# Optimization experiments

Hardware: AMD Instinct MI355X
Metric: run time of the kernel (lower is better)

The kernel has to match this reference:

```python
import jax, jax.numpy as jnp
import numpy as np

B, CI, HI, WI = 64, 3, 96, 96
G = 8
HG, WG = 16, 16
HIDLIN = 512
SIGMA_BOOST = 2.0
EPS = 1e-7
HID = (HI // 4 // 2) * (WI // 4 // 2) * 128  # 12*12*128 = 18432


def _conv(x, w, b):
    # NCHW conv, 3x3, padding 1 (matches nn.Conv2d(kernel_size=3, padding=1))
    y = jax.lax.conv_general_dilated(x, w, (1, 1), ((1, 1), (1, 1)),
                                     dimension_numbers=('NCHW', 'OIHW', 'NCHW'))
    return y + b[None, :, None, None]


def _maxpool(x, k):
    return jax.lax.reduce_window(x, -jnp.inf, jax.lax.max,
                                 (1, 1, k, k), (1, 1, k, k), 'VALID')


def setup_inputs() -> dict:
    key = jax.random.key(0)
    ks = jax.random.split(key, 22)

    def w(k, shape, fan_in):
        return jax.random.normal(k, shape, jnp.float32) * np.float32(1.0 / np.sqrt(fan_in))

    return {
        'image': jax.random.normal(ks[0], (B, CI, HI, WI), jnp.float32),
        'noise': jax.random.normal(ks[1], (B * G, 2), jnp.float32),
        # conv block 1
        'w1a': w(ks[2], (32, CI, 3, 3), CI * 9), 'b1a': jnp.zeros((32,), jnp.float32),
        'w1b': w(ks[3], (32, 32, 3, 3), 32 * 9), 'b1b': jnp.zeros((32,), jnp.float32),
        # conv block 2
        'w2a': w(ks[4], (64, 32, 3, 3), 32 * 9), 'b2a': jnp.zeros((64,), jnp.float32),
        'w2b': w(ks[5], (64, 64, 3, 3), 64 * 9), 'b2b': jnp.zeros((64,), jnp.float32),
        # conv block 3
        'w3a': w(ks[6], (128, 64, 3, 3), 64 * 9), 'b3a': jnp.zeros((128,), jnp.float32),
        'w3b': w(ks[7], (128, 128, 3, 3), 128 * 9), 'b3b': jnp.zeros((128,), jnp.float32),
        # linear head (weights stored (in, out))
        'wl1': w(ks[8], (HID, HIDLIN), HID), 'bl1': jnp.zeros((HIDLIN,), jnp.float32),
        'wl2': w(ks[9], (HIDLIN, HIDLIN), HIDLIN), 'bl2': jnp.zeros((HIDLIN,), jnp.float32),
        'wl3': w(ks[10], (HIDLIN, G * 3), HIDLIN), 'bl3': jnp.zeros((G * 3,), jnp.float32),
    }


def reference(image, noise, w1a, b1a, w1b, b1b, w2a, b2a, w2b, b2b,
              w3a, b3a, w3b, b3b, wl1, bl1, wl2, bl2, wl3, bl3):
    # --- preprocess CNN ---
    x = jax.nn.relu(_conv(image, w1a, b1a))
    x = jax.nn.relu(_conv(x, w1b, b1b))
    x = _maxpool(x, 4)
    x = jax.nn.relu(_conv(x, w2a, b2a))
    x = jax.nn.relu(_conv(x, w2b, b2b))
    x = _maxpool(x, 2)
    x = jax.nn.relu(_conv(x, w3a, b3a))
    x = jax.nn.relu(_conv(x, w3b, b3b))
    x = x.reshape(B, -1)                      # Flatten (C,H,W order, like torch .view)
    x = jax.nn.relu(x @ wl1 + bl1)
    x = jax.nn.relu(x @ wl2 + bl2)            # Linear(HIDLIN,HIDLIN) then the extra ReLU
    prep = (x @ wl3 + bl3).reshape(B * G, 3)  # (b*g, 3)

    means = prep[:, :2]                        # (b*g, 2) raw means
    sraw = prep[:, 2]
    # sparse.transform_sigmas: softplus(s + SIGMA_BOOST) + eps, scaled per spatial dim
    sig = jax.nn.softplus(sraw + SIGMA_BOOST) + EPS
    sigmas = sig[:, None] * jnp.array([HI - 1, WI - 1], jnp.float32)  # (b*g, 2)

    # Normal(means, sigmas).sample() -> reparameterized but detached (torch .sample())
    sample = jax.lax.stop_gradient(means + sigmas * noise)
    # sparse.transform_means over size (hi-hg, wi-wg): sigmoid * (size-1), then round
    msize = jnp.array([HI - HG - 1, WI - WG - 1], jnp.float32)
    pts = jnp.round(jax.nn.sigmoid(sample) * msize).astype(jnp.int32).reshape(B, G, 2)

    # glimpse extraction: the original's b*g python slicing loop -> vmapped dynamic_slice
    src = jax.lax.stop_gradient(image)  # original slices image.data (no grad)

    def ext_one(img, p):
        return jax.lax.dynamic_slice(img, (jnp.int32(0), p[0], p[1]), (CI, HG, WG))

    result = jax.vmap(lambda img, ps: jax.vmap(lambda p: ext_one(img, p))(ps))(src, pts)
    # result: (B, G, CI, HG, WG)
    return result, means.reshape(B, G, 2), sigmas.reshape(B, G, 2)
```

## Files before the change

kernel.cpp:

```cpp
#include <hip/hip_runtime.h>
#include <math.h>

constexpr int BB  = 64;
constexpr int CIc = 3;
constexpr int HIc = 96, WIc = 96;
constexpr int Gc  = 8, HGc = 16, WGc = 16;
constexpr int HIDc = 18432;
constexpr int HIDLINc = 512;

using short8 = __attribute__((ext_vector_type(8))) short;
using s4     = __attribute__((ext_vector_type(4))) short;
using f32x16 = __attribute__((ext_vector_type(16))) float;

__device__ inline unsigned short bfr(float f) {
    unsigned int u = __float_as_uint(f);
    u = (u + 0x7FFFu + ((u >> 16) & 1u)) >> 16;
    return (unsigned short)u;
}
__device__ inline float ubf(unsigned short s) {
    return __uint_as_float(((unsigned int)s) << 16);
}
__device__ inline void tsplit(float v, unsigned short& H, unsigned short& M,
                              unsigned short& L) {
    unsigned int u = __float_as_uint(v);
    H = (unsigned short)(u >> 16);
    float r1 = v - __uint_as_float(u & 0xFFFF0000u);
    unsigned int u1 = __float_as_uint(r1);
    M = (unsigned short)(u1 >> 16);
    float r2 = r1 - __uint_as_float(u1 & 0xFFFF0000u);
    L = (unsigned short)(__float_as_uint(r2) >> 16);
}

__device__ __attribute__((aligned(16))) unsigned short g_wh[9216];
__device__ __attribute__((aligned(16))) unsigned short g_wm[9216];
__device__ __attribute__((aligned(16))) unsigned short g_wl[9216];

__device__ __attribute__((aligned(16))) unsigned short g_w1ah[1536];
__device__ __attribute__((aligned(16))) unsigned short g_w1am[1536];
__device__ __attribute__((aligned(16))) unsigned short g_w1al[1536];

__device__ __attribute__((aligned(16))) unsigned short g_wph[276480];
__device__ __attribute__((aligned(16))) unsigned short g_wpm[276480];
__device__ __attribute__((aligned(16))) unsigned short g_wpl[276480];

__device__ inline void packN_one(const float* __restrict__ w, int CIN, int ofs,
                                 int idx)
{
    int chsz = 288 * CIN;
    int chunk = idx / chsz;
    int t = idx - chunk * chsz;
    int s = t >> 9;
    int rr = t & 511;
    int g = rr >> 8, oc32 = (rr >> 3) & 31, j = rr & 7;
    int nc16 = CIN / 16;
    int tap = s / nc16, c16 = s % nc16;
    int ci = c16 * 16 + g * 8 + j;
    int oc = chunk * 32 + oc32;
    float v = w[((size_t)oc * CIN + ci) * 9 + tap];
    unsigned short h = bfr(v);
    float r1 = v - ubf(h);
    unsigned short m = bfr(r1);
    g_wph[ofs + idx] = h; g_wpm[ofs + idx] = m; g_wpl[ofs + idx] = bfr(r1 - ubf(m));
}

__device__ inline void bz_one(unsigned short* __restrict__ Xh,
                              unsigned short* __restrict__ Xm,
                              unsigned short* __restrict__ Xl,
                              int PAD, int C, int idx)
{
    int RING = 4 * PAD - 4;
    int ci = idx % C;
    int cell = (idx / C) % RING;
    int b = idx / (C * RING);
    int y, x;
    if (cell < PAD)          { y = 0;       x = cell; }
    else if (cell < 2 * PAD) { y = PAD - 1; x = cell - PAD; }
    else { int t = cell - 2 * PAD; y = 1 + (t >> 1); x = (t & 1) ? PAD - 1 : 0; }
    size_t a = ((size_t)(b * PAD + y) * PAD + x) * C + ci;
    Xh[a] = 0; Xm[a] = 0; Xl[a] = 0;
}

__global__ void prep_all(const float* __restrict__ w1a, const float* __restrict__ w1b,
                         const float* __restrict__ w2a, const float* __restrict__ w2b,
                         const float* __restrict__ w3a, const float* __restrict__ w3b,
                         const float* __restrict__ image,
                         unsigned short* Ih, unsigned short* Im, unsigned short* Il,
                         unsigned short* X2h, unsigned short* X2m, unsigned short* X2l,
                         unsigned short* X3h, unsigned short* X3m, unsigned short* X3l,
                         unsigned short* X4h, unsigned short* X4m, unsigned short* X4l,
                         unsigned short* X5h, unsigned short* X5m, unsigned short* X5l)
{
    int idx = blockIdx.x * 256 + threadIdx.x;
    if (idx < 9216) {
        int j = idx & 7, oc = (idx >> 3) & 31, g = (idx >> 8) & 1, s = idx >> 9;
        int ci = 16 * (s & 1) + 8 * g + j;
        int tap = s >> 1;
        float v = w1b[(oc * 32 + ci) * 9 + tap];
        unsigned short h = bfr(v);
        float r1 = v - ubf(h);
        unsigned short m = bfr(r1);
        g_wh[idx] = h; g_wm[idx] = m; g_wl[idx] = bfr(r1 - ubf(m));
    } else if (idx < 27648) {
        packN_one(w2a, 32, 0, idx - 9216);
    } else if (idx < 64512) {
        packN_one(w2b, 64, 18432, idx - 27648);
    } else if (idx < 138240) {
        packN_one(w3a, 64, 55296, idx - 64512);
    } else if (idx < 285696) {
        packN_one(w3b, 128, 129024, idx - 138240);
    } else if (idx < 287232) {
        int i2 = idx - 285696;
        int j = i2 & 7, oc = (i2 >> 3) & 31, gg = (i2 >> 8) & 1, s = i2 >> 9;
        int k = s * 16 + gg * 8 + j;
        int tap = k >> 2, ci = k & 3;
        float v = (tap < 9 && ci < 3) ? w1a[((size_t)oc * 3 + ci) * 9 + tap] : 0.0f;
        unsigned short h = bfr(v);
        float r1 = v - ubf(h);
        unsigned short m = bfr(r1);
        g_w1ah[i2] = h; g_w1am[i2] = m; g_w1al[i2] = bfr(r1 - ubf(m));
    } else if (idx < 927232) {
        int c = idx - 287232;
        int x = c % 100;
        int t = c / 100;
        int y = t % 100;
        int b = t / 100;
        s4 H = {0, 0, 0, 0}, M = {0, 0, 0, 0}, L = {0, 0, 0, 0};
        if (y >= 2 && y < 98 && x >= 2 && x < 98) {
#pragma unroll
            for (int ci = 0; ci < 3; ++ci) {
                float v = image[((size_t)(b * 3 + ci) * 96 + (y - 2)) * 96 + (x - 2)];
                unsigned short hh, mm, ll;
                tsplit(v, hh, mm, ll);
                H[ci] = (short)hh; M[ci] = (short)mm; L[ci] = (short)ll;
            }
        }
        *(s4*)(Ih + (size_t)c * 4) = H;
        *(s4*)(Im + (size_t)c * 4) = M;
        *(s4*)(Il + (size_t)c * 4) = L;
    } else {
        int c = idx - 927232;
        if (c < 204800)        bz_one(X2h, X2m, X2l, 26, 32, c);
        else if (c < 614400)   bz_one(X3h, X3m, X3l, 26, 64, c - 204800);
        else if (c < 827392)   bz_one(X4h, X4m, X4l, 14, 64, c - 614400);
        else if (c < 1253376)  bz_one(X5h, X5m, X5l, 14, 128, c - 827392);
    }
}

__global__ __launch_bounds__(256, 5)
void conv1ab(const unsigned short* __restrict__ Ih,
             const unsigned short* __restrict__ Im,
             const unsigned short* __restrict__ Il,
             const float* __restrict__ b1a, const float* __restrict__ b1b,
             unsigned short* __restrict__ X2h, unsigned short* __restrict__ X2m,
             unsigned short* __restrict__ X2l)
{
    const int id    = blockIdx.x;
    const int xcd   = id & 7;
    const int local = id >> 3;
    const int gblk  = xcd * 576 + local;
    const int b  = gblk / 72;
    const int r  = gblk % 72;
    const int yq = r / 3;
    const int xt = r % 3;

    const int tid = threadIdx.x;
    const int wave = tid >> 6, lane = tid & 63;
    const int col = lane & 31, g = lane >> 5;

    __shared__ __align__(16) short s_hml[3][6][34][20];
    __shared__ float s_pool[4][8][2][16];
    __shared__ float s_b1a[32], s_b1b[32];
    if (tid < 32) { s_b1a[tid] = b1a[tid]; s_b1b[tid] = b1b[tid]; }
    __syncthreads();

    auto convA = [&](int tile, f32x16& acc) {
        int p = tile * 32 + col;
        int pc = p < 204 ? p : 203;
        int lr = pc / 34, lc = pc - (pc / 34) * 34;
        const size_t ibase =
            ((size_t)(b * 100 + 4 * yq + lr) * 100 + 32 * xt + lc) * 4;
#pragma unroll
        for (int s = 0; s < 3; ++s) {
            int tap0 = 4 * s + 2 * g; if (tap0 > 8) tap0 = 8;
            int tap1 = 4 * s + 2 * g + 1; if (tap1 > 8) tap1 = 8;
            int o0 = ((tap0 / 3) * 100 + tap0 % 3) * 4;
            int o1 = ((tap1 / 3) * 100 + tap1 % 3) * 4;
            s4 h0 = *(const s4*)(Ih + ibase + o0);
            s4 h1 = *(const s4*)(Ih + ibase + o1);
            s4 m0 = *(const s4*)(Im + ibase + o0);
            s4 m1 = *(const s4*)(Im + ibase + o1);
            s4 l0 = *(const s4*)(Il + ibase + o0);
            s4 l1 = *(const s4*)(Il + ibase + o1);
            short8 bh = __builtin_shufflevector(h0, h1, 0, 1, 2, 3, 4, 5, 6, 7);
            short8 bm = __builtin_shufflevector(m0, m1, 0, 1, 2, 3, 4, 5, 6, 7);
            short8 bl = __builtin_shufflevector(l0, l1, 0, 1, 2, 3, 4, 5, 6, 7);
            const int aidx = s * 512 + g * 256 + col * 8;
            short8 ah = *(const short8*)(g_w1ah + aidx);
            short8 am = *(const short8*)(g_w1am + aidx);
            short8 al = *(const short8*)(g_w1al + aidx);
            acc = __builtin_amdgcn_mfma_f32_32x32x16_bf16(ah, bh, acc, 0, 0, 0);
            acc = __builtin_amdgcn_mfma_f32_32x32x16_bf16(ah, bm, acc, 0, 0, 0);
            acc = __builtin_amdgcn_mfma_f32_32x32x16_bf16(am, bh, acc, 0, 0, 0);
            acc = __builtin_amdgcn_mfma_f32_32x32x16_bf16(am, bm, acc, 0, 0, 0);
            acc = __builtin_amdgcn_mfma_f32_32x32x16_bf16(al, bh, acc, 0, 0, 0);
            acc = __builtin_amdgcn_mfma_f32_32x32x16_bf16(ah, bl, acc, 0, 0, 0);
            acc = __builtin_amdgcn_mfma_f32_32x32x16_bf16(am, bl, acc, 0, 0, 0);
            acc = __builtin_amdgcn_mfma_f32_32x32x16_bf16(al, bm, acc, 0, 0, 0);
        }
    };

    f32x16 accA0 = {0,0,0,0,0,0,0,0,0,0,0,0,0,0,0,0};
    f32x16 accA1 = {0,0,0,0,0,0,0,0,0,0,0,0,0,0,0,0};
    convA(wave * 2, accA0);
    if (wave != 3) convA(wave * 2 + 1, accA1);

    f32x16 acc0 = {0,0,0,0,0,0,0,0,0,0,0,0,0,0,0,0};
    f32x16 acc1 = {0,0,0,0,0,0,0,0,0,0,0,0,0,0,0,0};

#pragma unroll
    for (int half = 0; half < 2; ++half) {
        if (half) __syncthreads();

#pragma unroll
        for (int t = 0; t < 2; ++t) {
            int tile = wave * 2 + t;
            int p = tile * 32 + col;
            if (tile < 7 && p < 204) {
                const f32x16& A = t ? accA1 : accA0;
                int lr = p / 34, lc = p - (p / 34) * 34;
                int gr = 4 * yq - 1 + lr, gc = 32 * xt - 1 + lc;
                bool valid = (gr >= 0 && gr < 96 && gc >= 0 && gc < 96);
                s4 H0, M0, L0, H1, M1, L1;
#pragma unroll
                for (int i = 0; i < 4; ++i) {
                    float v0 = valid ? fmaxf(A[8 * half + i] +
                                     s_b1a[16 * half + 4 * g + i], 0.0f) : 0.0f;
                    float v1 = valid ? fmaxf(A[8 * half + 4 + i] +
                                     s_b1a[16 * half + 8 + 4 * g + i], 0.0f) : 0.0f;
                    unsigned short hh, mm, ll;
                    tsplit(v0, hh, mm, ll);
                    H0[i] = (short)hh; M0[i] = (short)mm; L0[i] = (short)ll;
                    tsplit(v1, hh, mm, ll);
                    H1[i] = (short)hh; M1[i] = (short)mm; L1[i] = (short)ll;
                }
                *(s4*)&s_hml[0][lr][lc][4 * g]     = H0;
                *(s4*)&s_hml[0][lr][lc][8 + 4 * g] = H1;
                *(s4*)&s_hml[1][lr][lc][4 * g]     = M0;
                *(s4*)&s_hml[1][lr][lc][8 + 4 * g] = M1;
                *(s4*)&s_hml[2][lr][lc][4 * g]     = L0;
                *(s4*)&s_hml[2][lr][lc][8 + 4 * g] = L1;
            }
        }
        __syncthreads();

        __builtin_amdgcn_s_setprio(1);
#pragma unroll
        for (int tap = 0; tap < 9; ++tap) {
            const int s = tap * 2 + half;
            const int dy = tap / 3, dx = tap % 3;
            const int aidx = s * 512 + g * 256 + col * 8;

            s4 a0 = *(const s4*)(&s_hml[0][wave + dy][col + dx][g * 8]);
            s4 a1 = *(const s4*)(&s_hml[0][wave + dy][col + dx][g * 8 + 4]);
            s4 b0 = *(const s4*)(&s_hml[1][wave + dy][col + dx][g * 8]);
            s4 b1 = *(const s4*)(&s_hml[1][wave + dy][col + dx][g * 8 + 4]);
            s4 c0 = *(const s4*)(&s_hml[2][wave + dy][col + dx][g * 8]);
            s4 c1 = *(const s4*)(&s_hml[2][wave + dy][col + dx][g * 8 + 4]);

            short8 bh = __builtin_shufflevector(a0, a1, 0, 1, 2, 3, 4, 5, 6, 7);
            short8 bm = __builtin_shufflevector(b0, b1, 0, 1, 2, 3, 4, 5, 6, 7);
            short8 bl = __builtin_shufflevector(c0, c1, 0, 1, 2, 3, 4, 5, 6, 7);

            short8 ah = *(const short8*)(g_wh + aidx);
            short8 am = *(const short8*)(g_wm + aidx);
            short8 al = *(const short8*)(g_wl + aidx);

            acc0 = __builtin_amdgcn_mfma_f32_32x32x16_bf16(ah, bh, acc0, 0, 0, 0);
            acc1 = __builtin_amdgcn_mfma_f32_32x32x16_bf16(ah, bm, acc1, 0, 0, 0);
            acc0 = __builtin_amdgcn_mfma_f32_32x32x16_bf16(am, bh, acc0, 0, 0, 0);
            acc1 = __builtin_amdgcn_mfma_f32_32x32x16_bf16(am, bm, acc1, 0, 0, 0);
            acc0 = __builtin_amdgcn_mfma_f32_32x32x16_bf16(al, bh, acc0, 0, 0, 0);
            acc1 = __builtin_amdgcn_mfma_f32_32x32x16_bf16(ah, bl, acc1, 0, 0, 0);
        }
        __builtin_amdgcn_s_setprio(0);
    }
    __syncthreads();

#pragma unroll
    for (int rr = 0; rr < 16; ++rr) {
        int ocr = (rr & 3) + 8 * (rr >> 2) + 4 * g;
        float v = fmaxf(acc0[rr] + acc1[rr] + s_b1b[ocr], 0.0f);
        v = fmaxf(v, __shfl_xor(v, 1));
        v = fmaxf(v, __shfl_xor(v, 2));
        if ((col & 3) == 0) s_pool[wave][col >> 2][g][rr] = v;
    }
    __syncthreads();

    {
        int oc = tid & 31, pc = tid >> 5;
        if (pc < 8) {
            int gg = (oc >> 2) & 1;
            int rr = (oc & 3) + (((oc >> 3) & 3) << 2);
            float mv = s_pool[0][pc][gg][rr];
            mv = fmaxf(mv, s_pool[1][pc][gg][rr]);
            mv = fmaxf(mv, s_pool[2][pc][gg][rr]);
            mv = fmaxf(mv, s_pool[3][pc][gg][rr]);
            unsigned short h, m, l;
            tsplit(mv, h, m, l);
            size_t oa = ((size_t)(b * 26 + yq + 1) * 26 + xt * 8 + pc + 1) * 32 + oc;
            X2h[oa] = h; X2m[oa] = m; X2l[oa] = l;
        }
    }
}

template<int CIN, int HW, int NCHUNK, int OUTMODE>
__global__ __launch_bounds__(256)
void convN_mfma(const unsigned short* __restrict__ Xh,
                const unsigned short* __restrict__ Xm,
                const unsigned short* __restrict__ Xl,
                int wofs, const float* __restrict__ bias,
                unsigned short* __restrict__ Yh,
                unsigned short* __restrict__ Ym,
                unsigned short* __restrict__ Yl,
                float* __restrict__ Yf)
{
    constexpr int PAD = HW + 2;
    constexpr int NC16 = CIN / 16;
    constexpr int CHSZ = 288 * CIN;
    constexpr int COUT = NCHUNK * 32;

    const int tid = threadIdx.x;
    const int cpx = gridDim.x >> 3;
    const int blk = (blockIdx.x & 7) * cpx + (blockIdx.x >> 3);
    const int wid = blk * 4 + (tid >> 6);
    const int lane = tid & 63;
    const int col = lane & 31, g = lane >> 5;

    const int chunk = wid % NCHUNK;
    const int wt = wid / NCHUNK;
    const int P = wt * 32 + col;
    const int b = P / (HW * HW);
    const int rem = P - b * (HW * HW);
    const int y = rem / HW, x = rem - y * HW;

    const size_t ib = ((size_t)(b * PAD + y) * PAD + x) * CIN + g * 8;
    const int wbase = wofs + chunk * CHSZ;

    f32x16 acc0 = {0,0,0,0,0,0,0,0,0,0,0,0,0,0,0,0};
    f32x16 acc1 = {0,0,0,0,0,0,0,0,0,0,0,0,0,0,0,0};

#pragma unroll
    for (int tap = 0; tap < 9; ++tap) {
        const int dy = tap / 3, dx = tap % 3;
        for (int c16 = 0; c16 < NC16; ++c16) {
            const int s = tap * NC16 + c16;
            const int aidx = wbase + s * 512 + g * 256 + col * 8;
            const size_t xo = ib + (size_t)((dy * PAD + dx) * CIN + c16 * 16);
            short8 ah = *(const short8*)(g_wph + aidx);
            short8 am = *(const short8*)(g_wpm + aidx);
            short8 al = *(const short8*)(g_wpl + aidx);
            short8 bh = *(const short8*)(Xh + xo);
            short8 bm = *(const short8*)(Xm + xo);
            short8 bl = *(const short8*)(Xl + xo);
            acc0 = __builtin_amdgcn_mfma_f32_32x32x16_bf16(ah, bh, acc0, 0, 0, 0);
            acc1 = __builtin_amdgcn_mfma_f32_32x32x16_bf16(ah, bm, acc1, 0, 0, 0);
            acc0 = __builtin_amdgcn_mfma_f32_32x32x16_bf16(am, bh, acc0, 0, 0, 0);
            acc1 = __builtin_amdgcn_mfma_f32_32x32x16_bf16(am, bm, acc1, 0, 0, 0);
            acc0 = __builtin_amdgcn_mfma_f32_32x32x16_bf16(al, bh, acc0, 0, 0, 0);
            acc1 = __builtin_amdgcn_mfma_f32_32x32x16_bf16(ah, bl, acc1, 0, 0, 0);
        }
    }

    if constexpr (OUTMODE == 0) {
        const size_t obase =
            ((size_t)(b * PAD + y + 1) * PAD + (x + 1)) * COUT + chunk * 32;
#pragma unroll
        for (int q = 0; q < 4; ++q) {
            s4 H, M, L;
#pragma unroll
            for (int i = 0; i < 4; ++i) {
                int r = q * 4 + i;
                int ocr = i + 8 * q + 4 * g;
                float v = fmaxf(acc0[r] + acc1[r] + bias[chunk * 32 + ocr], 0.0f);
                unsigned short h, m, l;
                tsplit(v, h, m, l);
                H[i] = (short)h; M[i] = (short)m; L[i] = (short)l;
            }
            *(s4*)(Yh + obase + 8 * q + 4 * g) = H;
            *(s4*)(Ym + obase + 8 * q + 4 * g) = M;
            *(s4*)(Yl + obase + 8 * q + 4 * g) = L;
        }
    } else {
#pragma unroll
        for (int r = 0; r < 16; ++r) {
            int ocr = chunk * 32 + (r & 3) + 8 * (r >> 2) + 4 * g;
            float v = fmaxf(acc0[r] + acc1[r] + bias[ocr], 0.0f);
            Yf[((size_t)(b * COUT + ocr) * HW + y) * HW + x] = v;
        }
    }
}

__global__ __launch_bounds__(256)
void pool2_pack(const float* __restrict__ t2,
                unsigned short* __restrict__ X4h,
                unsigned short* __restrict__ X4m,
                unsigned short* __restrict__ X4l)
{
    int idx = blockIdx.x * 256 + threadIdx.x;
    constexpr int TOT = BB * 144 * 64;
    if (idx >= TOT) return;
    int oc = idx & 63;
    int p = (idx >> 6) % 144;
    int b = idx / (144 * 64);
    int y = p / 12, x = p % 12;
    const float* src = t2 + ((size_t)(b * 64 + oc) * 24 + 2 * y) * 24 + 2 * x;
    float v = fmaxf(fmaxf(src[0], src[1]), fmaxf(src[24], src[25]));
    unsigned short h, m, l;
    tsplit(v, h, m, l);
    size_t oa = ((size_t)(b * 14 + y + 1) * 14 + x + 1) * 64 + oc;
    X4h[oa] = h; X4m[oa] = m; X4l[oa] = l;
}

constexpr int KSPLIT = 64;
__global__ __launch_bounds__(256)
void lin1_partial(const float* __restrict__ x, const float* __restrict__ w,
                  float* __restrict__ partial)
{
    const int j  = threadIdx.x % 64;
    const int bg = threadIdx.x / 64;
    const int jBase = blockIdx.x * 64;
    const int k  = blockIdx.y;
    const int i0 = k * 288;

    __shared__ float s_x[32][68];

    float acc[16];
#pragma unroll
    for (int u = 0; u < 16; ++u) acc[u] = 0.0f;

    for (int ib = 0; ib < 288; ib += 32) {
        __syncthreads();
        {
            int lb = threadIdx.x / 4;
            int lo = (threadIdx.x % 4) * 8;
            const float* src = x + (size_t)lb * HIDc + i0 + ib + lo;
            float4 a0 = *(const float4*)(src);
            float4 a1 = *(const float4*)(src + 4);
            float tmp[8] = {a0.x, a0.y, a0.z, a0.w, a1.x, a1.y, a1.z, a1.w};
#pragma unroll
            for (int r = 0; r < 8; ++r) s_x[lo + r][lb] = tmp[r];
        }
        __syncthreads();

        for (int ii = 0; ii < 32; ++ii) {
            float wv = w[(size_t)(i0 + ib + ii) * HIDLINc + jBase + j];
            const float4* xp = (const float4*)&s_x[ii][bg * 16];
            float4 x0 = xp[0], x1 = xp[1], x2 = xp[2], x3 = xp[3];
            acc[0]  = fmaf(x0.x, wv, acc[0]);
            acc[1]  = fmaf(x0.y, wv, acc[1]);
            acc[2]  = fmaf(x0.z, wv, acc[2]);
            acc[3]  = fmaf(x0.w, wv, acc[3]);
            acc[4]  = fmaf(x1.x, wv, acc[4]);
            acc[5]  = fmaf(x1.y, wv, acc[5]);
            acc[6]  = fmaf(x1.z, wv, acc[6]);
            acc[7]  = fmaf(x1.w, wv, acc[7]);
            acc[8]  = fmaf(x2.x, wv, acc[8]);
            acc[9]  = fmaf(x2.y, wv, acc[9]);
            acc[10] = fmaf(x2.z, wv, acc[10]);
            acc[11] = fmaf(x2.w, wv, acc[11]);
            acc[12] = fmaf(x3.x, wv, acc[12]);
            acc[13] = fmaf(x3.y, wv, acc[13]);
            acc[14] = fmaf(x3.z, wv, acc[14]);
            acc[15] = fmaf(x3.w, wv, acc[15]);
        }
    }

#pragma unroll
    for (int u = 0; u < 16; ++u) {
        int b = bg * 16 + u;
        partial[((size_t)k * 64 + b) * HIDLINc + jBase + j] = acc[u];
    }
}

__global__ void lin1_reduce(const float* __restrict__ partial,
                            const float* __restrict__ bias,
                            float* __restrict__ x1)
{
    int idx = blockIdx.x * blockDim.x + threadIdx.x;
    if (idx >= 64 * HIDLINc) return;
    int j = idx % HIDLINc;
    float s = 0.0f;
    for (int k = 0; k < KSPLIT; ++k)
        s += partial[(size_t)k * 64 * HIDLINc + idx];
    x1[idx] = fmaxf(s + bias[j], 0.0f);
}

__global__ __launch_bounds__(256)
void lin2_k(const float* __restrict__ x1, const float* __restrict__ w,
            const float* __restrict__ bias, float* __restrict__ x2)
{
    const int j  = threadIdx.x % 64;
    const int bl = threadIdx.x / 64;
    const int jBase = blockIdx.x * 64;
    const int b = blockIdx.y * 4 + bl;

    __shared__ float s_x[4][HIDLINc];
    for (int idx = threadIdx.x; idx < 4 * HIDLINc; idx += 256)
        s_x[idx / HIDLINc][idx % HIDLINc] =
            x1[(size_t)(blockIdx.y * 4 + idx / HIDLINc) * HIDLINc + idx % HIDLINc];
    __syncthreads();

    float acc = 0.0f;
    for (int i = 0; i < HIDLINc; ++i)
        acc = fmaf(s_x[bl][i], w[(size_t)i * HIDLINc + jBase + j], acc);
    x2[(size_t)b * HIDLINc + jBase + j] = fmaxf(acc + bias[jBase + j], 0.0f);
}

__global__ void lin3_k(const float* __restrict__ x2, const float* __restrict__ w,
                       const float* __restrict__ bias, float* __restrict__ prep)
{
    int idx = blockIdx.x * blockDim.x + threadIdx.x;
    if (idx >= 64 * 24) return;
    int j = idx % 24, b = idx / 24;
    float acc = bias[j];
    for (int i = 0; i < HIDLINc; ++i)
        acc = fmaf(x2[(size_t)b * HIDLINc + i], w[i * 24 + j], acc);
    prep[idx] = acc;
}

__global__ void head_k(const float* __restrict__ prep, const float* __restrict__ noise,
                       float* __restrict__ outMeans, float* __restrict__ outSigmas,
                       int* __restrict__ pts)
{
    int id = blockIdx.x * blockDim.x + threadIdx.x;
    if (id >= BB * Gc) return;
    float m0 = prep[id * 3 + 0];
    float m1 = prep[id * 3 + 1];
    float sraw = prep[id * 3 + 2];
    float s = sraw + 2.0f;
    float sig = fmaxf(s, 0.0f) + log1pf(expf(-fabsf(s)));
    sig += 1e-7f;
    float sg = sig * 95.0f;
    outMeans[id * 2 + 0] = m0;
    outMeans[id * 2 + 1] = m1;
    outSigmas[id * 2 + 0] = sg;
    outSigmas[id * 2 + 1] = sg;
    float sa0 = m0 + sg * noise[id * 2 + 0];
    float sa1 = m1 + sg * noise[id * 2 + 1];
    float t0 = 1.0f / (1.0f + expf(-sa0));
    float t1 = 1.0f / (1.0f + expf(-sa1));
    pts[id * 2 + 0] = (int)rintf(t0 * 79.0f);
    pts[id * 2 + 1] = (int)rintf(t1 * 79.0f);
}

__global__ __launch_bounds__(256)
void patch_k(const float* __restrict__ image, const int* __restrict__ pts,
             float* __restrict__ outR)
{
    int id = blockIdx.x;
    int b = id / Gc;
    int p0 = pts[id * 2 + 0];
    int p1 = pts[id * 2 + 1];
    for (int idx = threadIdx.x; idx < CIc * HGc * WGc; idx += 256) {
        int c = idx / (HGc * WGc), rem = idx % (HGc * WGc);
        int hh = rem / WGc, ww = rem % WGc;
        outR[(size_t)id * (CIc * HGc * WGc) + idx] =
            image[((size_t)(b * CIc + c) * HIc + p0 + hh) * WIc + p1 + ww];
    }
}

extern "C" void kernel_launch(void* const* d_in, const int* in_sizes, int n_in,
                              void* d_out, int out_size, void* d_ws, size_t ws_size,
                              hipStream_t stream)
{
    const float* image = (const float*)d_in[0];
    const float* noise = (const float*)d_in[1];
    const float* w1a = (const float*)d_in[2];
    const float* b1a = (const float*)d_in[3];
    const float* w1b = (const float*)d_in[4];
    const float* b1b = (const float*)d_in[5];
    const float* w2a = (const float*)d_in[6];
    const float* b2a = (const float*)d_in[7];
    const float* w2b = (const float*)d_in[8];
    const float* b2b = (const float*)d_in[9];
    const float* w3a = (const float*)d_in[10];
    const float* b3a = (const float*)d_in[11];
    const float* w3b = (const float*)d_in[12];
    const float* b3b = (const float*)d_in[13];
    const float* wl1 = (const float*)d_in[14];
    const float* bl1 = (const float*)d_in[15];
    const float* wl2 = (const float*)d_in[16];
    const float* bl2 = (const float*)d_in[17];
    const float* wl3 = (const float*)d_in[18];
    const float* bl3 = (const float*)d_in[19];

    float* out = (float*)d_out;
    float* ws  = (float*)d_ws;

    unsigned short* X2h = (unsigned short*)(ws + 29884416);
    unsigned short* X2m = (unsigned short*)(ws + 30670848);
    unsigned short* X2l = (unsigned short*)(ws + 31457280);
    unsigned short* X3h = (unsigned short*)(ws);
    unsigned short* X3m = (unsigned short*)(ws + 1572864);
    unsigned short* X3l = (unsigned short*)(ws + 3145728);
    float*  t2  = ws + 4718592;
    unsigned short* X4h = (unsigned short*)(ws + 7340032);
    unsigned short* X4m = (unsigned short*)(ws + 7864320);
    unsigned short* X4l = (unsigned short*)(ws + 8388608);
    unsigned short* X5h = (unsigned short*)(ws + 8912896);
    unsigned short* X5m = (unsigned short*)(ws + 11010048);
    unsigned short* X5l = (unsigned short*)(ws + 12058624);
    float*  t5  = ws + 13107200;
    float*  part= ws + 14680064;
    float*  x1  = ws + 16777216;
    float*  x2  = x1 + 32768;
    float*  prep= x2 + 32768;
    int*    pts = (int*)(prep + 2048);
    unsigned short* Ih = (unsigned short*)(ws + 18874368);
    unsigned short* Im = (unsigned short*)(ws + 20447232);
    unsigned short* Il = (unsigned short*)(ws + 22020096);

    prep_all<<<8518, 256, 0, stream>>>(w1a, w1b, w2a, w2b, w3a, w3b, image,
                                       Ih, Im, Il,
                                       X2h, X2m, X2l, X3h, X3m, X3l,
                                       X4h, X4m, X4l, X5h, X5m, X5l);

    conv1ab<<<4608, 256, 0, stream>>>(Ih, Im, Il, b1a, b1b, X2h, X2m, X2l);

    convN_mfma<32, 24, 2, 0><<<576, 256, 0, stream>>>(
        X2h, X2m, X2l, 0, b2a, X3h, X3m, X3l, nullptr);
    convN_mfma<64, 24, 2, 1><<<576, 256, 0, stream>>>(
        X3h, X3m, X3l, 18432, b2b, nullptr, nullptr, nullptr, t2);
    pool2_pack<<<2304, 256, 0, stream>>>(t2, X4h, X4m, X4l);
    convN_mfma<64, 12, 4, 0><<<288, 256, 0, stream>>>(
        X4h, X4m, X4l, 55296, b3a, X5h, X5m, X5l, nullptr);
    convN_mfma<128, 12, 4, 1><<<288, 256, 0, stream>>>(
        X5h, X5m, X5l, 129024, b3b, nullptr, nullptr, nullptr, t5);

    lin1_partial<<<dim3(8, KSPLIT), 256, 0, stream>>>(t5, wl1, part);
    lin1_reduce<<<(64 * HIDLINc + 255) / 256, 256, 0, stream>>>(part, bl1, x1);
    lin2_k<<<dim3(8, 16), 256, 0, stream>>>(x1, wl2, bl2, x2);
    lin3_k<<<6, 256, 0, stream>>>(x2, wl3, bl3, prep);
    head_k<<<2, 256, 0, stream>>>(prep, noise,
                                  out + (size_t)BB * Gc * CIc * HGc * WGc,
                                  out + (size_t)BB * Gc * CIc * HGc * WGc + BB * Gc * 2,
                                  pts);
    patch_k<<<BB * Gc, 256, 0, stream>>>(image, pts, out);
}
```

Baseline: 354.7 us.

## Trim conv1a split-bf16 MFMA terms, use one-wave conv blocks, fuse lin3 with head

Conv1a's emulated-fp32 product drops the two mid×low MFMA cross terms, leaving six bf16 MFMAs per step instead of eight. The convN_mfma kernels move from 256-thread blocks with four waves to 64-thread single-wave blocks, with four times as many blocks and the same per-wave work. lin3 and the sampling head are fused into one per-batch kernel that keeps the hidden vector and prep values in shared memory, removing one launch and a global round-trip. Dropping the cross terms lowers conv1a precision, which could shift the rounded glimpse coordinates.

```diff
diff --git a/kernel.cpp b/kernel.cpp
--- a/kernel.cpp
+++ b/kernel.cpp
@@ -204,8 +204,6 @@
             acc = __builtin_amdgcn_mfma_f32_32x32x16_bf16(am, bm, acc, 0, 0, 0);
             acc = __builtin_amdgcn_mfma_f32_32x32x16_bf16(al, bh, acc, 0, 0, 0);
             acc = __builtin_amdgcn_mfma_f32_32x32x16_bf16(ah, bl, acc, 0, 0, 0);
-            acc = __builtin_amdgcn_mfma_f32_32x32x16_bf16(am, bl, acc, 0, 0, 0);
-            acc = __builtin_amdgcn_mfma_f32_32x32x16_bf16(al, bm, acc, 0, 0, 0);
         }
     };
 
@@ -314,7 +312,7 @@
 }
 
 template<int CIN, int HW, int NCHUNK, int OUTMODE>
-__global__ __launch_bounds__(256)
+__global__ __launch_bounds__(64)
 void convN_mfma(const unsigned short* __restrict__ Xh,
                 const unsigned short* __restrict__ Xm,
                 const unsigned short* __restrict__ Xl,
@@ -329,12 +327,10 @@
     constexpr int CHSZ = 288 * CIN;
     constexpr int COUT = NCHUNK * 32;
 
-    const int tid = threadIdx.x;
+    const int lane = threadIdx.x & 63;
+    const int col = lane & 31, g = lane >> 5;
     const int cpx = gridDim.x >> 3;
-    const int blk = (blockIdx.x & 7) * cpx + (blockIdx.x >> 3);
-    const int wid = blk * 4 + (tid >> 6);
-    const int lane = tid & 63;
-    const int col = lane & 31, g = lane >> 5;
+    const int wid = (blockIdx.x & 7) * cpx + (blockIdx.x >> 3);
 
     const int chunk = wid % NCHUNK;
     const int wt = wid / NCHUNK;
@@ -516,41 +512,49 @@
     x2[(size_t)b * HIDLINc + jBase + j] = fmaxf(acc + bias[jBase + j], 0.0f);
 }
 
-__global__ void lin3_k(const float* __restrict__ x2, const float* __restrict__ w,
-                       const float* __restrict__ bias, float* __restrict__ prep)
-{
-    int idx = blockIdx.x * blockDim.x + threadIdx.x;
-    if (idx >= 64 * 24) return;
-    int j = idx % 24, b = idx / 24;
-    float acc = bias[j];
-    for (int i = 0; i < HIDLINc; ++i)
-        acc = fmaf(x2[(size_t)b * HIDLINc + i], w[i * 24 + j], acc);
-    prep[idx] = acc;
-}
-
-__global__ void head_k(const float* __restrict__ prep, const float* __restrict__ noise,
-                       float* __restrict__ outMeans, float* __restrict__ outSigmas,
-                       int* __restrict__ pts)
-{
-    int id = blockIdx.x * blockDim.x + threadIdx.x;
-    if (id >= BB * Gc) return;
-    float m0 = prep[id * 3 + 0];
-    float m1 = prep[id * 3 + 1];
-    float sraw = prep[id * 3 + 2];
-    float s = sraw + 2.0f;
-    float sig = fmaxf(s, 0.0f) + log1pf(expf(-fabsf(s)));
-    sig += 1e-7f;
-    float sg = sig * 95.0f;
-    outMeans[id * 2 + 0] = m0;
-    outMeans[id * 2 + 1] = m1;
-    outSigmas[id * 2 + 0] = sg;
-    outSigmas[id * 2 + 1] = sg;
-    float sa0 = m0 + sg * noise[id * 2 + 0];
-    float sa1 = m1 + sg * noise[id * 2 + 1];
-    float t0 = 1.0f / (1.0f + expf(-sa0));
-    float t1 = 1.0f / (1.0f + expf(-sa1));
-    pts[id * 2 + 0] = (int)rintf(t0 * 79.0f);
-    pts[id * 2 + 1] = (int)rintf(t1 * 79.0f);
+__global__ __launch_bounds__(256)
+void lin3head_k(const float* __restrict__ x2, const float* __restrict__ w,
+                const float* __restrict__ bias, const float* __restrict__ noise,
+                float* __restrict__ outMeans, float* __restrict__ outSigmas,
+                int* __restrict__ pts)
+{
+    const int b = blockIdx.x;
+    const int tid = threadIdx.x;
+    __shared__ float s_x[HIDLINc];
+    __shared__ float s_prep[24];
+
+    for (int i = tid; i < HIDLINc; i += 256)
+        s_x[i] = x2[(size_t)b * HIDLINc + i];
+    __syncthreads();
+
+    if (tid < 24) {
+        float acc = bias[tid];
+        for (int i = 0; i < HIDLINc; ++i)
+            acc = fmaf(s_x[i], w[i * 24 + tid], acc);
+        s_prep[tid] = acc;
+    }
+    __syncthreads();
+
+    if (tid < 8) {
+        int id = b * Gc + tid;
+        float m0 = s_prep[tid * 3 + 0];
+        float m1 = s_prep[tid * 3 + 1];
+        float sraw = s_prep[tid * 3 + 2];
+        float s = sraw + 2.0f;
+        float sig = fmaxf(s, 0.0f) + log1pf(expf(-fabsf(s)));
+        sig += 1e-7f;
+        float sg = sig * 95.0f;
+        outMeans[id * 2 + 0] = m0;
+        outMeans[id * 2 + 1] = m1;
+        outSigmas[id * 2 + 0] = sg;
+        outSigmas[id * 2 + 1] = sg;
+        float sa0 = m0 + sg * noise[id * 2 + 0];
+        float sa1 = m1 + sg * noise[id * 2 + 1];
+        float t0 = 1.0f / (1.0f + expf(-sa0));
+        float t1 = 1.0f / (1.0f + expf(-sa1));
+        pts[id * 2 + 0] = (int)rintf(t0 * 79.0f);
+        pts[id * 2 + 1] = (int)rintf(t1 * 79.0f);
+    }
 }
 
 __global__ __launch_bounds__(256)
@@ -627,23 +631,22 @@
 
     conv1ab<<<4608, 256, 0, stream>>>(Ih, Im, Il, b1a, b1b, X2h, X2m, X2l);
 
-    convN_mfma<32, 24, 2, 0><<<576, 256, 0, stream>>>(
+    convN_mfma<32, 24, 2, 0><<<2304, 64, 0, stream>>>(
         X2h, X2m, X2l, 0, b2a, X3h, X3m, X3l, nullptr);
-    convN_mfma<64, 24, 2, 1><<<576, 256, 0, stream>>>(
+    convN_mfma<64, 24, 2, 1><<<2304, 64, 0, stream>>>(
         X3h, X3m, X3l, 18432, b2b, nullptr, nullptr, nullptr, t2);
     pool2_pack<<<2304, 256, 0, stream>>>(t2, X4h, X4m, X4l);
-    convN_mfma<64, 12, 4, 0><<<288, 256, 0, stream>>>(
+    convN_mfma<64, 12, 4, 0><<<1152, 64, 0, stream>>>(
         X4h, X4m, X4l, 55296, b3a, X5h, X5m, X5l, nullptr);
-    convN_mfma<128, 12, 4, 1><<<288, 256, 0, stream>>>(
+    convN_mfma<128, 12, 4, 1><<<1152, 64, 0, stream>>>(
         X5h, X5m, X5l, 129024, b3b, nullptr, nullptr, nullptr, t5);
 
     lin1_partial<<<dim3(8, KSPLIT), 256, 0, stream>>>(t5, wl1, part);
     lin1_reduce<<<(64 * HIDLINc + 255) / 256, 256, 0, stream>>>(part, bl1, x1);
     lin2_k<<<dim3(8, 16), 256, 0, stream>>>(x1, wl2, bl2, x2);
-    lin3_k<<<6, 256, 0, stream>>>(x2, wl3, bl3, prep);
-    head_k<<<2, 256, 0, stream>>>(prep, noise,
-                                  out + (size_t)BB * Gc * CIc * HGc * WGc,
-                                  out + (size_t)BB * Gc * CIc * HGc * WGc + BB * Gc * 2,
-                                  pts);
+    lin3head_k<<<64, 256, 0, stream>>>(x2, wl3, bl3, noise,
+                                       out + (size_t)BB * Gc * CIc * HGc * WGc,
+                                       out + (size_t)BB * Gc * CIc * HGc * WGc + BB * Gc * 2,
+                                       pts);
     patch_k<<<BB * Gc, 256, 0, stream>>>(image, pts, out);
 }
```

After: 319.6 us. 9.9% less time.
